# Performance work log

Hardware: AMD Instinct MI355X
Metric: run time of the kernel (lower is better)

## Reference

```python
import jax, jax.numpy as jnp
import numpy as np
import math

FEAT = 128
HEADS = 4
HEAD_DIM = FEAT // HEADS
SEQ = 32
NODES = 20000
LN_EPS = 1e-5


def setup_inputs() -> dict:
    key = jax.random.key(0)
    ks = jax.random.split(key, 16)
    s = 1.0 / math.sqrt(FEAT)
    inp = {
        "query": jax.random.normal(ks[0], (NODES, FEAT), jnp.float32),
        "key": jax.random.normal(ks[1], (SEQ, NODES, FEAT), jnp.float32),
        "value": jax.random.normal(ks[2], (SEQ, NODES, FEAT), jnp.float32),
        "mask_idx": jax.random.randint(ks[3], (NODES,), 0, SEQ, jnp.int64 if jax.config.jax_enable_x64 else jnp.int32),
        "Wq": jax.random.normal(ks[4], (FEAT, FEAT), jnp.float32) * s,
        "bq": jnp.zeros((FEAT,), jnp.float32),
        "Wk": jax.random.normal(ks[5], (FEAT, FEAT), jnp.float32) * s,
        "bk": jnp.zeros((FEAT,), jnp.float32),
        "Wv": jax.random.normal(ks[6], (FEAT, FEAT), jnp.float32) * s,
        "bv": jnp.zeros((FEAT,), jnp.float32),
        "Wo": jax.random.normal(ks[7], (FEAT, FEAT), jnp.float32) * s,
        "bo": jnp.zeros((FEAT,), jnp.float32),
        "gamma": jnp.ones((FEAT,), jnp.float32),
        "beta": jnp.zeros((FEAT,), jnp.float32),
    }
    return inp


def reference(query, key, value, mask_idx, Wq, bq, Wk, bk, Wv, bv, Wo, bo, gamma, beta):
    S, N, F = key.shape
    H, D = HEADS, HEAD_DIM
    input_query = query
    q = (query @ Wq + bq).reshape(N, H, D)                      # [N,H,D]
    k = (key @ Wk + bk).transpose(1, 0, 2).reshape(N, S, H, D)  # [N,S,H,D]
    v = (value @ Wv + bv).transpose(1, 0, 2).reshape(N, S, H, D)
    scores = jnp.einsum('nhd,nshd->nsh', q, k) / math.sqrt(D)   # [N,S,H]
    # per-node ragged mask: positions >= mask_idx[n] are masked out
    pos = jnp.arange(S)[None, :]                                # [1,S]
    mask = (pos >= mask_idx[:, None]).astype(jnp.float32) * -1e9  # [N,S]
    scores = scores + mask[:, :, None]
    attn = jax.nn.softmax(scores, axis=1)                       # softmax over seq
    # dropout is identity in eval mode
    wv = jnp.einsum('nsh,nshd->nhd', attn, v).reshape(N, F)
    out = wv @ Wo + bo
    mu = jnp.mean(out, axis=-1, keepdims=True)
    var = jnp.mean(jnp.square(out - mu), axis=-1, keepdims=True)
    ln = (out - mu) / jnp.sqrt(var + LN_EPS) * gamma + beta
    return input_query + ln
```

## Files before the change

kernel.cpp:

```cpp
#include <hip/hip_runtime.h>

#define N_NODES 20000
#define FEAT    128
#define SEQ     32
#define HEADS   4
#define HDIM    32
#define NT      8
#define RS      132
#define SS      36

__device__ __forceinline__ void fma4(float4& a, float s, const float4 b) {
    a.x = fmaf(s, b.x, a.x);
    a.y = fmaf(s, b.y, a.y);
    a.z = fmaf(s, b.z, a.z);
    a.w = fmaf(s, b.w, a.w);
}

__global__ void transpose_wk(const float* __restrict__ Wk, float* __restrict__ WkT) {
    int tid = blockIdx.x * blockDim.x + threadIdx.x;
    int c = tid >> 7, f = tid & 127;
    WkT[c * 128 + f] = Wk[f * 128 + c];
}

__global__ __launch_bounds__(256) void mha_fused(
    const float* __restrict__ query, const float* __restrict__ key,
    const float* __restrict__ value, const int* __restrict__ mask_idx,
    const float* __restrict__ Wq, const float* __restrict__ bq,
    const float* __restrict__ WkT, const float* __restrict__ bk,
    const float* __restrict__ Wv, const float* __restrict__ bv,
    const float* __restrict__ Wo, const float* __restrict__ bo,
    const float* __restrict__ gamma, const float* __restrict__ beta,
    float* __restrict__ out)
{
    __shared__ float qT[NT * RS];
    __shared__ float qh[NT * RS];
    __shared__ float qk[NT * 4 * RS];
    __shared__ float sc[NT * 4 * SS];
    __shared__ float av[NT * 4 * RS];
    __shared__ float ot[NT * RS];
    __shared__ float qbk[NT * 4];

    const int tid   = threadIdx.x;
    const int node0 = blockIdx.x * NT;
    const int ng = tid >> 5;
    const int f4 = tid & 31;
    const int fo = f4 * 4;

    {
        int i  = tid * 4;
        int nd = i >> 7, f = i & 127;
        float4 v = *(const float4*)&query[(long)(node0 + nd) * FEAT + f];
        *(float4*)&qT[nd * RS + f] = v;
    }
    __syncthreads();

    {
        float4 acc = {0.f, 0.f, 0.f, 0.f};
        for (int c = 0; c < 128; ++c) {
            float qv = qT[ng * RS + c];
            float4 w = *(const float4*)&Wq[c * 128 + fo];
            fma4(acc, qv, w);
        }
        float4 b = *(const float4*)&bq[fo];
        acc.x += b.x; acc.y += b.y; acc.z += b.z; acc.w += b.w;
        *(float4*)&qh[ng * RS + fo] = acc;
    }
    __syncthreads();

    {
        float4 acc[4];
        #pragma unroll
        for (int h = 0; h < 4; ++h) acc[h] = make_float4(0.f, 0.f, 0.f, 0.f);
        for (int d = 0; d < 32; ++d) {
            #pragma unroll
            for (int h = 0; h < 4; ++h) {
                float qv = qh[ng * RS + h * 32 + d];
                float4 w = *(const float4*)&WkT[(h * 32 + d) * 128 + fo];
                fma4(acc[h], qv, w);
            }
        }
        #pragma unroll
        for (int h = 0; h < 4; ++h)
            *(float4*)&qk[(ng * 4 + h) * RS + fo] = acc[h];
    }
    if (tid < 32) {
        int nd = tid >> 2, h = tid & 3;
        float s = 0.f;
        for (int d = 0; d < 32; ++d)
            s = fmaf(qh[nd * RS + h * 32 + d], bk[h * 32 + d], s);
        qbk[nd * 4 + h] = s;
    }
    __syncthreads();

    {
        const int s  = tid >> 3;
        const int q8 = tid & 7;
        const long kbase = ((long)s * N_NODES + node0) * FEAT + q8 * 16;
        for (int nd = 0; nd < NT; ++nd) {
            const float4 k0 = *(const float4*)&key[kbase + nd * FEAT + 0];
            const float4 k1 = *(const float4*)&key[kbase + nd * FEAT + 4];
            const float4 k2 = *(const float4*)&key[kbase + nd * FEAT + 8];
            const float4 k3 = *(const float4*)&key[kbase + nd * FEAT + 12];
            #pragma unroll
            for (int h = 0; h < 4; ++h) {
                const float* qkp = &qk[(nd * 4 + h) * RS + q8 * 16];
                float4 a0 = *(const float4*)&qkp[0];
                float4 a1 = *(const float4*)&qkp[4];
                float4 a2 = *(const float4*)&qkp[8];
                float4 a3 = *(const float4*)&qkp[12];
                float p = 0.f;
                p = fmaf(k0.x, a0.x, p); p = fmaf(k0.y, a0.y, p);
                p = fmaf(k0.z, a0.z, p); p = fmaf(k0.w, a0.w, p);
                p = fmaf(k1.x, a1.x, p); p = fmaf(k1.y, a1.y, p);
                p = fmaf(k1.z, a1.z, p); p = fmaf(k1.w, a1.w, p);
                p = fmaf(k2.x, a2.x, p); p = fmaf(k2.y, a2.y, p);
                p = fmaf(k2.z, a2.z, p); p = fmaf(k2.w, a2.w, p);
                p = fmaf(k3.x, a3.x, p); p = fmaf(k3.y, a3.y, p);
                p = fmaf(k3.z, a3.z, p); p = fmaf(k3.w, a3.w, p);
                p += __shfl_xor(p, 1);
                p += __shfl_xor(p, 2);
                p += __shfl_xor(p, 4);
                if (q8 == 0) sc[(nd * 4 + h) * SS + s] = p;
            }
        }
    }
    __syncthreads();

    if (tid < 32) {
        const int nd = tid >> 2, h = tid & 3;
        const int mi = mask_idx[node0 + nd];
        const float qb = qbk[nd * 4 + h];
        const float scale = 0.17677669529663687f;
        float mx = -1e30f;
        for (int s2 = 0; s2 < 32; ++s2) {
            float v = (sc[(nd * 4 + h) * SS + s2] + qb) * scale;
            if (s2 >= mi) v += -1e9f;
            sc[(nd * 4 + h) * SS + s2] = v;
            mx = fmaxf(mx, v);
        }
        float sum = 0.f;
        for (int s2 = 0; s2 < 32; ++s2) {
            float e = __expf(sc[(nd * 4 + h) * SS + s2] - mx);
            sc[(nd * 4 + h) * SS + s2] = e;
            sum += e;
        }
        const float inv = 1.f / sum;
        for (int s2 = 0; s2 < 32; ++s2)
            sc[(nd * 4 + h) * SS + s2] *= inv;
    }
    __syncthreads();

    {
        float4 acc[4];
        #pragma unroll
        for (int h = 0; h < 4; ++h) acc[h] = make_float4(0.f, 0.f, 0.f, 0.f);
        const long vbase = (long)(node0 + ng) * FEAT + fo;
        for (int s2 = 0; s2 < 32; ++s2) {
            float4 vv = *(const float4*)&value[vbase + (long)s2 * N_NODES * FEAT];
            #pragma unroll
            for (int h = 0; h < 4; ++h) {
                float a = sc[(ng * 4 + h) * SS + s2];
                fma4(acc[h], a, vv);
            }
        }
        #pragma unroll
        for (int h = 0; h < 4; ++h)
            *(float4*)&av[(ng * 4 + h) * RS + fo] = acc[h];
    }
    __syncthreads();

    {
        const int h = fo >> 5;
        float4 acc = {0.f, 0.f, 0.f, 0.f};
        for (int f = 0; f < 128; ++f) {
            float a = av[(ng * 4 + h) * RS + f];
            float4 w = *(const float4*)&Wv[f * 128 + fo];
            fma4(acc, a, w);
        }
        float4 b = *(const float4*)&bv[fo];
        acc.x += b.x; acc.y += b.y; acc.z += b.z; acc.w += b.w;
        *(float4*)&qh[ng * RS + fo] = acc;
    }
    __syncthreads();

    {
        float4 acc = {0.f, 0.f, 0.f, 0.f};
        for (int c = 0; c < 128; ++c) {
            float wvv = qh[ng * RS + c];
            float4 w = *(const float4*)&Wo[c * 128 + fo];
            fma4(acc, wvv, w);
        }
        float4 b = *(const float4*)&bo[fo];
        acc.x += b.x; acc.y += b.y; acc.z += b.z; acc.w += b.w;
        *(float4*)&ot[ng * RS + fo] = acc;
    }
    __syncthreads();

    {
        float4 x = *(float4*)&ot[ng * RS + fo];
        float s1 = x.x + x.y + x.z + x.w;
        float s2 = x.x * x.x + x.y * x.y + x.z * x.z + x.w * x.w;
        #pragma unroll
        for (int off = 1; off < 32; off <<= 1) {
            s1 += __shfl_xor(s1, off);
            s2 += __shfl_xor(s2, off);
        }
        const float mu  = s1 * (1.f / 128.f);
        const float var = s2 * (1.f / 128.f) - mu * mu;
        const float rstd = rsqrtf(var + 1e-5f);
        float4 g = *(const float4*)&gamma[fo];
        float4 b = *(const float4*)&beta[fo];
        float4 q = *(float4*)&qT[ng * RS + fo];
        float4 r;
        r.x = (x.x - mu) * rstd * g.x + b.x + q.x;
        r.y = (x.y - mu) * rstd * g.y + b.y + q.y;
        r.z = (x.z - mu) * rstd * g.z + b.z + q.z;
        r.w = (x.w - mu) * rstd * g.w + b.w + q.w;
        *(float4*)&out[(long)(node0 + ng) * FEAT + fo] = r;
    }
}

extern "C" void kernel_launch(void* const* d_in, const int* in_sizes, int n_in,
                              void* d_out, int out_size, void* d_ws, size_t ws_size,
                              hipStream_t stream) {
    const float* query = (const float*)d_in[0];
    const float* key   = (const float*)d_in[1];
    const float* value = (const float*)d_in[2];
    const int*   midx  = (const int*)  d_in[3];
    const float* Wq    = (const float*)d_in[4];
    const float* bq    = (const float*)d_in[5];
    const float* Wk    = (const float*)d_in[6];
    const float* bk    = (const float*)d_in[7];
    const float* Wv    = (const float*)d_in[8];
    const float* bv    = (const float*)d_in[9];
    const float* Wo    = (const float*)d_in[10];
    const float* bo    = (const float*)d_in[11];
    const float* gamma = (const float*)d_in[12];
    const float* beta  = (const float*)d_in[13];

    float* WkT = (float*)d_ws;

    transpose_wk<<<64, 256, 0, stream>>>(Wk, WkT);
    mha_fused<<<N_NODES / NT, 256, 0, stream>>>(
        query, key, value, midx, Wq, bq, WkT, bk, Wv, bv, Wo, bo,
        gamma, beta, (float*)d_out);
}
```

Measured before the change: 785.4 us.

## Skip masked key/value positions and parallelize softmax across lanes

Reads each node's mask length once and skips loading keys and values for sequence positions beyond it, since their softmax weights underflow to zero. Fully masked nodes still use all positions to match the uniform-softmax behaviour. Softmax is split across 8 lanes per head with shuffle reductions, and shared buffers are merged to cut LDS usage, with a minimum occupancy hint added. Risks include divergence from ragged lengths and exactness that relies on the underflow.

```diff
diff --git a/kernel.cpp b/kernel.cpp
--- a/kernel.cpp
+++ b/kernel.cpp
@@ -22,7 +22,7 @@
     WkT[c * 128 + f] = Wk[f * 128 + c];
 }
 
-__global__ __launch_bounds__(256) void mha_fused(
+__global__ __launch_bounds__(256, 5) void mha_fused(
     const float* __restrict__ query, const float* __restrict__ key,
     const float* __restrict__ value, const int* __restrict__ mask_idx,
     const float* __restrict__ Wq, const float* __restrict__ bq,
@@ -34,11 +34,11 @@
 {
     __shared__ float qT[NT * RS];
     __shared__ float qh[NT * RS];
-    __shared__ float qk[NT * 4 * RS];
+    __shared__ float qkav[NT * 4 * RS];
     __shared__ float sc[NT * 4 * SS];
-    __shared__ float av[NT * 4 * RS];
-    __shared__ float ot[NT * RS];
     __shared__ float qbk[NT * 4];
+    __shared__ int   Ls[NT];
+    __shared__ int   Mi[NT];
 
     const int tid   = threadIdx.x;
     const int node0 = blockIdx.x * NT;
@@ -51,6 +51,11 @@
         int nd = i >> 7, f = i & 127;
         float4 v = *(const float4*)&query[(long)(node0 + nd) * FEAT + f];
         *(float4*)&qT[nd * RS + f] = v;
+        if (tid < NT) {
+            int m = mask_idx[node0 + tid];
+            Mi[tid] = m;
+            Ls[tid] = (m == 0) ? SEQ : m;
+        }
     }
     __syncthreads();
 
@@ -81,14 +86,14 @@
         }
         #pragma unroll
         for (int h = 0; h < 4; ++h)
-            *(float4*)&qk[(ng * 4 + h) * RS + fo] = acc[h];
+            *(float4*)&qkav[(ng * 4 + h) * RS + fo] = acc[h];
     }
     if (tid < 32) {
         int nd = tid >> 2, h = tid & 3;
         float s = 0.f;
         for (int d = 0; d < 32; ++d)
             s = fmaf(qh[nd * RS + h * 32 + d], bk[h * 32 + d], s);
-        qbk[nd * 4 + h] = s;
+        qbk[tid] = s;
     }
     __syncthreads();
 
@@ -97,56 +102,75 @@
         const int q8 = tid & 7;
         const long kbase = ((long)s * N_NODES + node0) * FEAT + q8 * 16;
         for (int nd = 0; nd < NT; ++nd) {
-            const float4 k0 = *(const float4*)&key[kbase + nd * FEAT + 0];
-            const float4 k1 = *(const float4*)&key[kbase + nd * FEAT + 4];
-            const float4 k2 = *(const float4*)&key[kbase + nd * FEAT + 8];
-            const float4 k3 = *(const float4*)&key[kbase + nd * FEAT + 12];
-            #pragma unroll
-            for (int h = 0; h < 4; ++h) {
-                const float* qkp = &qk[(nd * 4 + h) * RS + q8 * 16];
-                float4 a0 = *(const float4*)&qkp[0];
-                float4 a1 = *(const float4*)&qkp[4];
-                float4 a2 = *(const float4*)&qkp[8];
-                float4 a3 = *(const float4*)&qkp[12];
-                float p = 0.f;
-                p = fmaf(k0.x, a0.x, p); p = fmaf(k0.y, a0.y, p);
-                p = fmaf(k0.z, a0.z, p); p = fmaf(k0.w, a0.w, p);
-                p = fmaf(k1.x, a1.x, p); p = fmaf(k1.y, a1.y, p);
-                p = fmaf(k1.z, a1.z, p); p = fmaf(k1.w, a1.w, p);
-                p = fmaf(k2.x, a2.x, p); p = fmaf(k2.y, a2.y, p);
-                p = fmaf(k2.z, a2.z, p); p = fmaf(k2.w, a2.w, p);
-                p = fmaf(k3.x, a3.x, p); p = fmaf(k3.y, a3.y, p);
-                p = fmaf(k3.z, a3.z, p); p = fmaf(k3.w, a3.w, p);
-                p += __shfl_xor(p, 1);
-                p += __shfl_xor(p, 2);
-                p += __shfl_xor(p, 4);
-                if (q8 == 0) sc[(nd * 4 + h) * SS + s] = p;
+            if (s < Ls[nd]) {
+                const float4 k0 = *(const float4*)&key[kbase + nd * FEAT + 0];
+                const float4 k1 = *(const float4*)&key[kbase + nd * FEAT + 4];
+                const float4 k2 = *(const float4*)&key[kbase + nd * FEAT + 8];
+                const float4 k3 = *(const float4*)&key[kbase + nd * FEAT + 12];
+                #pragma unroll
+                for (int h = 0; h < 4; ++h) {
+                    const float* qkp = &qkav[(nd * 4 + h) * RS + q8 * 16];
+                    float4 a0 = *(const float4*)&qkp[0];
+                    float4 a1 = *(const float4*)&qkp[4];
+                    float4 a2 = *(const float4*)&qkp[8];
+                    float4 a3 = *(const float4*)&qkp[12];
+                    float p = 0.f;
+                    p = fmaf(k0.x, a0.x, p); p = fmaf(k0.y, a0.y, p);
+                    p = fmaf(k0.z, a0.z, p); p = fmaf(k0.w, a0.w, p);
+                    p = fmaf(k1.x, a1.x, p); p = fmaf(k1.y, a1.y, p);
+                    p = fmaf(k1.z, a1.z, p); p = fmaf(k1.w, a1.w, p);
+                    p = fmaf(k2.x, a2.x, p); p = fmaf(k2.y, a2.y, p);
+                    p = fmaf(k2.z, a2.z, p); p = fmaf(k2.w, a2.w, p);
+                    p = fmaf(k3.x, a3.x, p); p = fmaf(k3.y, a3.y, p);
+                    p = fmaf(k3.z, a3.z, p); p = fmaf(k3.w, a3.w, p);
+                    p += __shfl_xor(p, 1);
+                    p += __shfl_xor(p, 2);
+                    p += __shfl_xor(p, 4);
+                    if (q8 == 0) sc[(nd * 4 + h) * SS + s] = p;
+                }
             }
         }
     }
     __syncthreads();
 
-    if (tid < 32) {
-        const int nd = tid >> 2, h = tid & 3;
-        const int mi = mask_idx[node0 + nd];
-        const float qb = qbk[nd * 4 + h];
+    {
+        const int pair  = tid >> 3;
+        const int lane8 = tid & 7;
+        const int nd = pair >> 2;
+        const int L  = Ls[nd];
+        const bool mi0 = (Mi[nd] == 0);
+        const float qb = qbk[pair];
         const float scale = 0.17677669529663687f;
-        float mx = -1e30f;
-        for (int s2 = 0; s2 < 32; ++s2) {
-            float v = (sc[(nd * 4 + h) * SS + s2] + qb) * scale;
-            if (s2 >= mi) v += -1e9f;
-            sc[(nd * 4 + h) * SS + s2] = v;
-            mx = fmaxf(mx, v);
-        }
-        float sum = 0.f;
-        for (int s2 = 0; s2 < 32; ++s2) {
-            float e = __expf(sc[(nd * 4 + h) * SS + s2] - mx);
-            sc[(nd * 4 + h) * SS + s2] = e;
-            sum += e;
-        }
+        float v[4];
+        #pragma unroll
+        for (int i = 0; i < 4; ++i) {
+            int s2 = lane8 * 4 + i;
+            if (s2 < L) {
+                float t = (sc[pair * SS + s2] + qb) * scale;
+                if (mi0) t += -1e9f;
+                v[i] = t;
+            } else v[i] = -3.0e38f;
+        }
+        float mx = fmaxf(fmaxf(v[0], v[1]), fmaxf(v[2], v[3]));
+        mx = fmaxf(mx, __shfl_xor(mx, 1));
+        mx = fmaxf(mx, __shfl_xor(mx, 2));
+        mx = fmaxf(mx, __shfl_xor(mx, 4));
+        float e[4], sum = 0.f;
+        #pragma unroll
+        for (int i = 0; i < 4; ++i) {
+            int s2 = lane8 * 4 + i;
+            e[i] = (s2 < L) ? __expf(v[i] - mx) : 0.f;
+            sum += e[i];
+        }
+        sum += __shfl_xor(sum, 1);
+        sum += __shfl_xor(sum, 2);
+        sum += __shfl_xor(sum, 4);
         const float inv = 1.f / sum;
-        for (int s2 = 0; s2 < 32; ++s2)
-            sc[(nd * 4 + h) * SS + s2] *= inv;
+        #pragma unroll
+        for (int i = 0; i < 4; ++i) {
+            int s2 = lane8 * 4 + i;
+            if (s2 < L) sc[pair * SS + s2] = e[i] * inv;
+        }
     }
     __syncthreads();
 
@@ -155,7 +179,8 @@
         #pragma unroll
         for (int h = 0; h < 4; ++h) acc[h] = make_float4(0.f, 0.f, 0.f, 0.f);
         const long vbase = (long)(node0 + ng) * FEAT + fo;
-        for (int s2 = 0; s2 < 32; ++s2) {
+        const int L = Ls[ng];
+        for (int s2 = 0; s2 < L; ++s2) {
             float4 vv = *(const float4*)&value[vbase + (long)s2 * N_NODES * FEAT];
             #pragma unroll
             for (int h = 0; h < 4; ++h) {
@@ -163,9 +188,10 @@
                 fma4(acc[h], a, vv);
             }
         }
+        __syncthreads();
         #pragma unroll
         for (int h = 0; h < 4; ++h)
-            *(float4*)&av[(ng * 4 + h) * RS + fo] = acc[h];
+            *(float4*)&qkav[(ng * 4 + h) * RS + fo] = acc[h];
     }
     __syncthreads();
 
@@ -173,31 +199,27 @@
         const int h = fo >> 5;
         float4 acc = {0.f, 0.f, 0.f, 0.f};
         for (int f = 0; f < 128; ++f) {
-            float a = av[(ng * 4 + h) * RS + f];
+            float a = qkav[(ng * 4 + h) * RS + f];
             float4 w = *(const float4*)&Wv[f * 128 + fo];
             fma4(acc, a, w);
         }
         float4 b = *(const float4*)&bv[fo];
         acc.x += b.x; acc.y += b.y; acc.z += b.z; acc.w += b.w;
+        __syncthreads();
         *(float4*)&qh[ng * RS + fo] = acc;
     }
     __syncthreads();
 
     {
-        float4 acc = {0.f, 0.f, 0.f, 0.f};
+        float4 x = {0.f, 0.f, 0.f, 0.f};
         for (int c = 0; c < 128; ++c) {
             float wvv = qh[ng * RS + c];
             float4 w = *(const float4*)&Wo[c * 128 + fo];
-            fma4(acc, wvv, w);
+            fma4(x, wvv, w);
         }
         float4 b = *(const float4*)&bo[fo];
-        acc.x += b.x; acc.y += b.y; acc.z += b.z; acc.w += b.w;
-        *(float4*)&ot[ng * RS + fo] = acc;
-    }
-    __syncthreads();
-
-    {
-        float4 x = *(float4*)&ot[ng * RS + fo];
+        x.x += b.x; x.y += b.y; x.z += b.z; x.w += b.w;
+
         float s1 = x.x + x.y + x.z + x.w;
         float s2 = x.x * x.x + x.y * x.y + x.z * x.z + x.w * x.w;
         #pragma unroll
@@ -209,13 +231,13 @@
         const float var = s2 * (1.f / 128.f) - mu * mu;
         const float rstd = rsqrtf(var + 1e-5f);
         float4 g = *(const float4*)&gamma[fo];
-        float4 b = *(const float4*)&beta[fo];
+        float4 bt = *(const float4*)&beta[fo];
         float4 q = *(float4*)&qT[ng * RS + fo];
         float4 r;
-        r.x = (x.x - mu) * rstd * g.x + b.x + q.x;
-        r.y = (x.y - mu) * rstd * g.y + b.y + q.y;
-        r.z = (x.z - mu) * rstd * g.z + b.z + q.z;
-        r.w = (x.w - mu) * rstd * g.w + b.w + q.w;
+        r.x = (x.x - mu) * rstd * g.x + bt.x + q.x;
+        r.y = (x.y - mu) * rstd * g.y + bt.y + q.y;
+        r.z = (x.z - mu) * rstd * g.z + bt.z + q.z;
+        r.w = (x.w - mu) * rstd * g.w + bt.w + q.w;
         *(float4*)&out[(long)(node0 + ng) * FEAT + fo] = r;
     }
 }
```

Result: faster. 719.2 us (-8.4%).
